# Kernel tuning notes

Measured on AMD Instinct MI355X. Metric: run time of the kernel, lower is better.

Reference implementation:

```python
import jax, jax.numpy as jnp
import numpy as np

R, C, N, E, H, F, ED, G, L = 1, 4, 50000, 200000, 128, 128, 16, 64, 2


def setup_inputs() -> dict:
    key = jax.random.key(0)
    ks = jax.random.split(key, 16)
    s = 0.05
    return {
        "x": jax.random.normal(ks[0], (R * C * N, H), jnp.float32),
        "batch": jnp.sort(jax.random.randint(ks[1], (N,), 0, G)),
        "edge_index": jax.random.randint(ks[2], (2, E), 0, N),
        "edge_attr": jax.random.normal(ks[3], (1, 1, E, ED), jnp.float32),
        "node_mask": jax.random.uniform(ks[4], (R, C, N, 1), jnp.float32),
        "edge_mask": jax.random.uniform(ks[5], (R, C, E, 1), jnp.float32),
        "W_be": jax.random.normal(ks[6], (ED, H), jnp.float32) * s,
        "b_be": jnp.zeros((H,), jnp.float32),
        "eps": jnp.zeros((L,), jnp.float32),
        "W1": jax.random.normal(ks[7], (L, H, H), jnp.float32) * s,
        "b1": jnp.zeros((L, H), jnp.float32),
        "W2": jax.random.normal(ks[8], (L, H, H), jnp.float32) * s,
        "b2": jnp.zeros((L, H), jnp.float32),
        "Wm1": jax.random.normal(ks[9], (H, H), jnp.float32) * s,
        "bm1": jnp.zeros((H,), jnp.float32),
        "Wm2": jax.random.normal(ks[10], (H, F), jnp.float32) * s,
        "bm2": jnp.zeros((F,), jnp.float32),
    }


def reference(x, batch, edge_index, edge_attr, node_mask, edge_mask,
              W_be, b_be, eps, W1, b1, W2, b2, Wm1, bm1, Wm2, bm2):
    gelu = lambda v: jax.nn.gelu(v, approximate=False)  # torch F.gelu default is erf
    src, dst = edge_index[0], edge_index[1]
    # bond encoder, shared across conv layers: (1,1,E,H)
    ee = edge_attr @ W_be + b_be
    for l in range(L):
        ux = x.reshape(R, C, N, H)
        # gather + add + GELU + edge-weight multiply: (R,C,E,H)
        msg = gelu(ux[:, :, src, :] + ee) * edge_mask
        # scatter_sum over edges into destination nodes
        agg = jnp.zeros_like(ux).at[:, :, dst, :].add(msg)
        h = (1.0 + eps[l]) * x + agg.reshape(x.shape)
        # conv MLP: Linear -> GELU -> Linear, then outer GELU (norm=Identity, dropout=0)
        h = gelu(h @ W1[l] + b1[l]) @ W2[l] + b2[l]
        x = gelu(h)
    # final node MLP (PyG MLP, norm=None): Linear -> GELU -> Linear
    x = gelu(x @ Wm1 + bm1) @ Wm2 + bm2  # (R*C*N, F)
    x4 = x.reshape(R, C, N, F)
    # masked mean-pool per (repeat, centroid, graph)
    num = jnp.zeros((R, C, G, F), x.dtype).at[:, :, batch, :].add(x4 * node_mask)
    den = jnp.zeros((R, C, G, 1), x.dtype).at[:, :, batch, :].add(node_mask) + 1e-7
    pooled = (num / den).transpose(0, 2, 1, 3).reshape(-1, F)  # (R*G*C, F)
    return pooled
```

## Files before the change

### kernel.cpp

```cpp
#include <hip/hip_runtime.h>
#include <math.h>

#define NN 50000
#define EN 200000
#define CC 4
#define HH 128
#define GG 64
#define LDSA 136
#define LDSF 132

typedef __attribute__((ext_vector_type(8))) short bs8;
typedef __attribute__((ext_vector_type(4))) float f32x4;
typedef __attribute__((ext_vector_type(2))) float f32x2;

__device__ __forceinline__ unsigned short f2bf(float f) {
  unsigned int u = __float_as_uint(f);
  u += 0x7FFFu + ((u >> 16) & 1u);
  return (unsigned short)(u >> 16);
}
__device__ __forceinline__ float bf2f(unsigned short h) {
  return __uint_as_float(((unsigned int)h) << 16);
}
__device__ __forceinline__ float gelu_f(float x) {
  float z = fabsf(x) * 0.7071067811865476f;
  float t = __builtin_amdgcn_rcpf(fmaf(0.3275911f, z, 1.0f));
  float poly = t * fmaf(t, fmaf(t, fmaf(t, fmaf(t, 1.061405429f, -1.453152027f),
                                        1.421413741f), -0.284496736f), 0.254829592f);
  float e = fmaf(-poly, __expf(-z * z), 1.0f);
  return 0.5f * x * (1.0f + copysignf(e, x));
}
__device__ __forceinline__ float gelu2_f(float x) {
  float z = fabsf(x) * 0.7071067811865476f;
  float t = __builtin_amdgcn_rcpf(fmaf(0.3275911f, z, 1.0f));
  float poly = t * fmaf(t, fmaf(t, fmaf(t, fmaf(t, 1.061405429f, -1.453152027f),
                                        1.421413741f), -0.284496736f), 0.254829592f);
  float e = fmaf(-poly, __expf(-z * z), 1.0f);
  return x * (1.0f + copysignf(e, x));
}

__global__ __launch_bounds__(256) void count_kernel(const int* __restrict__ dst,
                                                    int* __restrict__ counts) {
  int e = blockIdx.x * 256 + threadIdx.x;
  if (e < EN) atomicAdd(&counts[dst[e]], 1);
}

__global__ __launch_bounds__(256) void block_sum_kernel(const int* __restrict__ counts,
                                                        int* __restrict__ bsums) {
  int tid = threadIdx.x;
  int i = blockIdx.x * 256 + tid;
  int v = (i < NN) ? counts[i] : 0;
#pragma unroll
  for (int d = 1; d < 64; d <<= 1) v += __shfl_xor(v, d);
  __shared__ int ws4[4];
  if ((tid & 63) == 0) ws4[tid >> 6] = v;
  __syncthreads();
  if (tid == 0) bsums[blockIdx.x] = ws4[0] + ws4[1] + ws4[2] + ws4[3];
}

__global__ __launch_bounds__(256) void bsum_scan_kernel(const int* __restrict__ bsums,
                                                        int* __restrict__ boffs, int nb) {
  int tid = threadIdx.x, lane = tid & 63, wv = tid >> 6;
  int v = (tid < nb) ? bsums[tid] : 0;
  int s = v;
#pragma unroll
  for (int d = 1; d < 64; d <<= 1) { int t = __shfl_up(s, d); if (lane >= d) s += t; }
  __shared__ int wsum[4];
  if (lane == 63) wsum[wv] = s;
  __syncthreads();
  int pre = 0;
  for (int j = 0; j < wv; ++j) pre += wsum[j];
  if (tid < nb) boffs[tid] = pre + s - v;
}

__global__ __launch_bounds__(256) void block_scan_kernel(const int* __restrict__ counts,
                                                         const int* __restrict__ boffs,
                                                         int* __restrict__ offsets,
                                                         int* __restrict__ cursor) {
  int tid = threadIdx.x, lane = tid & 63, wv = tid >> 6;
  int i = blockIdx.x * 256 + tid;
  int v = (i < NN) ? counts[i] : 0;
  int s = v;
#pragma unroll
  for (int d = 1; d < 64; d <<= 1) { int t = __shfl_up(s, d); if (lane >= d) s += t; }
  __shared__ int wsum[4];
  if (lane == 63) wsum[wv] = s;
  __syncthreads();
  int pre = boffs[blockIdx.x];
  for (int j = 0; j < wv; ++j) pre += wsum[j];
  if (i < NN) { int e = pre + s - v; offsets[i] = e; cursor[i] = e; }
  if (i == 0) offsets[NN] = EN;
}

__global__ __launch_bounds__(256) void fill_kernel(const int* __restrict__ dst,
                                                   const int* __restrict__ src,
                                                   const float* __restrict__ emask,
                                                   int* __restrict__ cursor,
                                                   int2* __restrict__ csr_es,
                                                   float4* __restrict__ emask_s) {
  int e = blockIdx.x * 256 + threadIdx.x;
  if (e < EN) {
    int s = src[e];
    float m0 = emask[e];
    float m1 = emask[EN + e];
    float m2 = emask[2 * EN + e];
    float m3 = emask[3 * EN + e];
    int pos = atomicAdd(&cursor[dst[e]], 1);
    csr_es[pos] = make_int2(e, s);
    emask_s[pos] = make_float4(m0, m1, m2, m3);
  }
}

__global__ __launch_bounds__(256) void prep_w_kernel(const float* __restrict__ W1,
                                                     const float* __restrict__ W2,
                                                     const float* __restrict__ Wm1,
                                                     const float* __restrict__ Wm2,
                                                     unsigned short* __restrict__ wts) {
  int m = blockIdx.x >> 6;
  int idx = (blockIdx.x & 63) * 256 + threadIdx.x;
  const float* src = (m == 0) ? W1 : (m == 1) ? W1 + 16384 : (m == 2) ? W2
                     : (m == 3) ? W2 + 16384 : (m == 4) ? Wm1 : Wm2;
  unsigned short* dhi = wts + m * 32768;
  unsigned short* dlo = dhi + 16384;
  int n = idx >> 7, k = idx & 127;
  float v = src[k * HH + n];
  unsigned short hi = f2bf(v);
  dhi[n * HH + k] = hi;
  dlo[n * HH + k] = f2bf(v - bf2f(hi));
}

__global__ __launch_bounds__(256) void ee_kernel(const float* __restrict__ eattr,
                                                 const float* __restrict__ Wbe,
                                                 const float* __restrict__ bbe,
                                                 float* __restrict__ ee) {
  __shared__ float Ws[16 * HH];
  __shared__ float Ea[16 * 16];
  int tid = threadIdx.x;
  int e0 = blockIdx.x * 16;
#pragma unroll
  for (int i = 0; i < 8; ++i) Ws[tid + i * 256] = Wbe[tid + i * 256];
  Ea[tid] = eattr[(size_t)e0 * 16 + tid];
  __syncthreads();
  int h = tid & 127, half = tid >> 7;
  float bb = bbe[h];
#pragma unroll
  for (int j = 0; j < 8; ++j) {
    int el = j * 2 + half;
    float acc = bb;
#pragma unroll
    for (int d = 0; d < 16; ++d) acc += Ea[el * 16 + d] * Ws[d * HH + h];
    ee[(size_t)(e0 + el) * HH + h] = acc;
  }
}

__device__ __forceinline__ void loadW(const unsigned short* __restrict__ whi,
                                      const unsigned short* __restrict__ wlo,
                                      bs8 (&bh)[4][2], bs8 (&bl)[4][2],
                                      int ln, int quad, int wq) {
#pragma unroll
  for (int ks = 0; ks < 4; ++ks)
#pragma unroll
    for (int nt = 0; nt < 2; ++nt) {
      int wrow = ((wq * 2 + nt) * 16 + ln) * HH + ks * 32 + quad * 8;
      bh[ks][nt] = *(const bs8*)(whi + wrow);
      bl[ks][nt] = *(const bs8*)(wlo + wrow);
    }
}
__device__ __forceinline__ void zacc(f32x4 (&acc)[4][2]) {
#pragma unroll
  for (int mt = 0; mt < 4; ++mt)
#pragma unroll
    for (int nt = 0; nt < 2; ++nt)
#pragma unroll
      for (int r = 0; r < 4; ++r) acc[mt][nt][r] = 0.f;
}
__device__ __forceinline__ void gemm3(const unsigned short* Ahi, const unsigned short* Alo,
                                      const bs8 (&bh)[4][2], const bs8 (&bl)[4][2],
                                      f32x4 (&acc)[4][2], int ln, int quad) {
#pragma unroll
  for (int ks = 0; ks < 4; ++ks) {
    bs8 ah[4], al[4];
    int sb = ((ks * 4 + quad) ^ ln) * 8;
#pragma unroll
    for (int mt = 0; mt < 4; ++mt) {
      ah[mt] = *(const bs8*)(Ahi + (mt * 16 + ln) * HH + sb);
      al[mt] = *(const bs8*)(Alo + (mt * 16 + ln) * HH + sb);
    }
#pragma unroll
    for (int nt = 0; nt < 2; ++nt)
#pragma unroll
      for (int mt = 0; mt < 4; ++mt) {
        acc[mt][nt] = __builtin_amdgcn_mfma_f32_16x16x32_bf16(al[mt], bh[ks][nt], acc[mt][nt], 0, 0, 0);
        acc[mt][nt] = __builtin_amdgcn_mfma_f32_16x16x32_bf16(ah[mt], bl[ks][nt], acc[mt][nt], 0, 0, 0);
        acc[mt][nt] = __builtin_amdgcn_mfma_f32_16x16x32_bf16(ah[mt], bh[ks][nt], acc[mt][nt], 0, 0, 0);
      }
  }
}
__device__ __forceinline__ void tstage(unsigned short* Ahi, unsigned short* Alo,
                                       const float* __restrict__ b1v, f32x4 (&acc)[4][2],
                                       int ln, int quad, int wq) {
#pragma unroll
  for (int nt = 0; nt < 2; ++nt) {
    int col = (wq * 2 + nt) * 16 + ln;
    int cb = col >> 3, co = col & 7;
    float bb = b1v[col];
#pragma unroll
    for (int mt = 0; mt < 4; ++mt)
#pragma unroll
      for (int r = 0; r < 4; ++r) {
        float tv = gelu_f(acc[mt][nt][r] + bb);
        unsigned short th = f2bf(tv);
        int rr = mt * 16 + quad * 4 + r;
        int sof = rr * HH + (cb ^ (rr & 15)) * 8 + co;
        Ahi[sof] = th;
        Alo[sof] = f2bf(tv - bf2f(th));
      }
  }
}

__global__ __launch_bounds__(256, 4) void layer_kernel(
    const float* __restrict__ x,
    const float* __restrict__ ee,
    const int* __restrict__ off,
    const int2* __restrict__ csr_es,
    const float4* __restrict__ emask_s,
    const float* __restrict__ epsp, int layer,
    const unsigned short* __restrict__ w1hi, const unsigned short* __restrict__ w1lo,
    const float* __restrict__ b1,
    const unsigned short* __restrict__ w2hi, const unsigned short* __restrict__ w2lo,
    const float* __restrict__ b2,
    float* __restrict__ out) {
  __shared__ __align__(16) unsigned short AB[2 * 64 * HH];
  unsigned short* Ahi = AB;
  unsigned short* Alo = AB + 64 * HH;
  int tid = threadIdx.x;
  int lane = tid & 63, wq = tid >> 6;
  int ln = lane & 15, quad = lane >> 4;
  int n0 = blockIdx.x * 16;
  int c2 = lane * 2;
  float ep = 1.0f + epsp[layer];
  int blk = lane >> 2;
  int wo = (lane & 3) * 2;

  for (int j = 0; j < 4; ++j) {
    int nn = wq * 4 + j;
    int v = n0 + nn;
    float2 acc[CC];
#pragma unroll
    for (int c = 0; c < CC; ++c) { acc[c].x = 0.f; acc[c].y = 0.f; }
    int beg = off[v], end = off[v + 1];

    float2 eeC; float2 xC[CC]; float emC[CC];
    int2 esN = make_int2(0, 0);
    eeC.x = 0.f; eeC.y = 0.f;
#pragma unroll
    for (int c = 0; c < CC; ++c) { xC[c].x = 0.f; xC[c].y = 0.f; emC[c] = 0.f; }

    if (beg < end) {
      int2 es0 = csr_es[beg];
      eeC = *(const float2*)(ee + (size_t)es0.x * HH + c2);
#pragma unroll
      for (int c = 0; c < CC; ++c)
        xC[c] = *(const float2*)(x + ((size_t)c * NN + es0.y) * HH + c2);
      float4 m = emask_s[beg];
      emC[0] = 0.5f * m.x; emC[1] = 0.5f * m.y; emC[2] = 0.5f * m.z; emC[3] = 0.5f * m.w;
      if (beg + 1 < end) esN = csr_es[beg + 1];
    }

    for (int t = beg; t < end; ++t) {
      float2 eeB; float2 xB[CC]; float emB[CC];
      int2 esNN = make_int2(0, 0);
      if (t + 1 < end) {
        eeB = *(const float2*)(ee + (size_t)esN.x * HH + c2);
#pragma unroll
        for (int c = 0; c < CC; ++c)
          xB[c] = *(const float2*)(x + ((size_t)c * NN + esN.y) * HH + c2);
        float4 m = emask_s[t + 1];
        emB[0] = 0.5f * m.x; emB[1] = 0.5f * m.y; emB[2] = 0.5f * m.z; emB[3] = 0.5f * m.w;
        if (t + 2 < end) esNN = csr_es[t + 2];
      } else {
        eeB.x = 0.f; eeB.y = 0.f;
#pragma unroll
        for (int c = 0; c < CC; ++c) { xB[c].x = 0.f; xB[c].y = 0.f; emB[c] = 0.f; }
      }
#pragma unroll
      for (int c = 0; c < CC; ++c) {
        acc[c].x += gelu2_f(xC[c].x + eeC.x) * emC[c];
        acc[c].y += gelu2_f(xC[c].y + eeC.y) * emC[c];
      }
      eeC = eeB;
#pragma unroll
      for (int c = 0; c < CC; ++c) { xC[c] = xB[c]; emC[c] = emB[c]; }
      esN = esNN;
    }

#pragma unroll
    for (int c = 0; c < CC; ++c) {
      float2 xs = *(const float2*)(x + ((size_t)c * NN + v) * HH + c2);
      float o0 = fmaf(ep, xs.x, acc[c].x);
      float o1 = fmaf(ep, xs.y, acc[c].y);
      int rr = c * 16 + nn;
      int base = rr * HH + ((blk ^ (rr & 15)) * 8) + wo;
      unsigned short h0 = f2bf(o0), h1 = f2bf(o1);
      ushort2 hv; hv.x = h0; hv.y = h1;
      ushort2 lv; lv.x = f2bf(o0 - bf2f(h0)); lv.y = f2bf(o1 - bf2f(h1));
      *(ushort2*)(Ahi + base) = hv;
      *(ushort2*)(Alo + base) = lv;
    }
  }

  bs8 w1h[4][2], w1l[4][2];
  loadW(w1hi, w1lo, w1h, w1l, ln, quad, wq);
  __syncthreads();

  f32x4 acc[4][2];
  zacc(acc);
  gemm3(Ahi, Alo, w1h, w1l, acc, ln, quad);
  __syncthreads();

  bs8 w2h[4][2], w2l[4][2];
  loadW(w2hi, w2lo, w2h, w2l, ln, quad, wq);
  tstage(Ahi, Alo, b1, acc, ln, quad, wq);
  __syncthreads();

  zacc(acc);
  gemm3(Ahi, Alo, w2h, w2l, acc, ln, quad);

#pragma unroll
  for (int nt = 0; nt < 2; ++nt) {
    int col = (wq * 2 + nt) * 16 + ln;
    float bb = b2[col];
#pragma unroll
    for (int mt = 0; mt < 4; ++mt)
#pragma unroll
      for (int r = 0; r < 4; ++r) {
        float o = gelu_f(acc[mt][nt][r] + bb);
        out[((size_t)mt * NN + n0 + quad * 4 + r) * HH + col] = o;
      }
  }
}

__global__ __launch_bounds__(256, 2) void mlp_pool_kernel(
    const float* __restrict__ in,
    const unsigned short* __restrict__ w1hi, const unsigned short* __restrict__ w1lo,
    const float* __restrict__ b1,
    const unsigned short* __restrict__ w2hi, const unsigned short* __restrict__ w2lo,
    const float* __restrict__ b2,
    const float* __restrict__ nmask, const int* __restrict__ batch,
    float* __restrict__ num) {
  __shared__ __align__(16) unsigned short AB[128 * LDSA];
  __shared__ int kk[64];
  unsigned short* Ahi = AB;
  unsigned short* Alo = AB + 64 * LDSA;
  int tid = threadIdx.x;
  int row0 = blockIdx.x * 64;
  int lane = tid & 63, wq = tid >> 6;
  int ln = lane & 15, quad = lane >> 4;

  bs8 b1h[4][2], b1l[4][2];
  loadW(w1hi, w1lo, b1h, b1l, ln, quad, wq);
#pragma unroll
  for (int i = 0; i < 8; ++i) {
    int idx = tid + i * 256;
    int r = idx >> 5, cc4 = idx & 31;
    f32x4 vv = __builtin_nontemporal_load(
        (const f32x4*)(in + (size_t)(row0 + r) * HH + cc4 * 4));
    unsigned short h0 = f2bf(vv[0]), h1 = f2bf(vv[1]), h2 = f2bf(vv[2]), h3 = f2bf(vv[3]);
    ushort4 hv; hv.x = h0; hv.y = h1; hv.z = h2; hv.w = h3;
    ushort4 lv;
    lv.x = f2bf(vv[0] - bf2f(h0)); lv.y = f2bf(vv[1] - bf2f(h1));
    lv.z = f2bf(vv[2] - bf2f(h2)); lv.w = f2bf(vv[3] - bf2f(h3));
    *(ushort4*)(Ahi + r * LDSA + cc4 * 4) = hv;
    *(ushort4*)(Alo + r * LDSA + cc4 * 4) = lv;
  }
  if (tid < 64) {
    int gr = row0 + tid;
    int c = gr / NN;
    int n = gr - c * NN;
    kk[tid] = (c << 6) | batch[n];
  }
  __syncthreads();

  f32x4 acc[4][2];
  zacc(acc);
#pragma unroll
  for (int ks = 0; ks < 4; ++ks) {
    bs8 ah[4], al[4];
#pragma unroll
    for (int mt = 0; mt < 4; ++mt) {
      ah[mt] = *(const bs8*)(Ahi + (mt * 16 + ln) * LDSA + ks * 32 + quad * 8);
      al[mt] = *(const bs8*)(Alo + (mt * 16 + ln) * LDSA + ks * 32 + quad * 8);
    }
#pragma unroll
    for (int nt = 0; nt < 2; ++nt)
#pragma unroll
      for (int mt = 0; mt < 4; ++mt) {
        acc[mt][nt] = __builtin_amdgcn_mfma_f32_16x16x32_bf16(al[mt], b1h[ks][nt], acc[mt][nt], 0, 0, 0);
        acc[mt][nt] = __builtin_amdgcn_mfma_f32_16x16x32_bf16(ah[mt], b1l[ks][nt], acc[mt][nt], 0, 0, 0);
        acc[mt][nt] = __builtin_amdgcn_mfma_f32_16x16x32_bf16(ah[mt], b1h[ks][nt], acc[mt][nt], 0, 0, 0);
      }
  }
  __syncthreads();

  bs8 b2h[4][2], b2l[4][2];
  loadW(w2hi, w2lo, b2h, b2l, ln, quad, wq);
#pragma unroll
  for (int nt = 0; nt < 2; ++nt) {
    int col = (wq * 2 + nt) * 16 + ln;
    float bb = b1[col];
#pragma unroll
    for (int mt = 0; mt < 4; ++mt)
#pragma unroll
      for (int r = 0; r < 4; ++r) {
        float tv = gelu_f(acc[mt][nt][r] + bb);
        unsigned short th = f2bf(tv);
        int rr = mt * 16 + quad * 4 + r;
        Ahi[rr * LDSA + col] = th;
        Alo[rr * LDSA + col] = f2bf(tv - bf2f(th));
      }
  }
  __syncthreads();

  zacc(acc);
#pragma unroll
  for (int ks = 0; ks < 4; ++ks) {
    bs8 ah[4], al[4];
#pragma unroll
    for (int mt = 0; mt < 4; ++mt) {
      ah[mt] = *(const bs8*)(Ahi + (mt * 16 + ln) * LDSA + ks * 32 + quad * 8);
      al[mt] = *(const bs8*)(Alo + (mt * 16 + ln) * LDSA + ks * 32 + quad * 8);
    }
#pragma unroll
    for (int nt = 0; nt < 2; ++nt)
#pragma unroll
      for (int mt = 0; mt < 4; ++mt) {
        acc[mt][nt] = __builtin_amdgcn_mfma_f32_16x16x32_bf16(al[mt], b2h[ks][nt], acc[mt][nt], 0, 0, 0);
        acc[mt][nt] = __builtin_amdgcn_mfma_f32_16x16x32_bf16(ah[mt], b2l[ks][nt], acc[mt][nt], 0, 0, 0);
        acc[mt][nt] = __builtin_amdgcn_mfma_f32_16x16x32_bf16(ah[mt], b2h[ks][nt], acc[mt][nt], 0, 0, 0);
      }
  }
  __syncthreads();
  float* Tf = (float*)AB;
#pragma unroll
  for (int nt = 0; nt < 2; ++nt) {
    int col = (wq * 2 + nt) * 16 + ln;
    float bb = b2[col];
#pragma unroll
    for (int mt = 0; mt < 4; ++mt)
#pragma unroll
      for (int r = 0; r < 4; ++r) {
        int rl = mt * 16 + quad * 4 + r;
        int gr = row0 + rl;
        Tf[rl * LDSF + col] = (acc[mt][nt][r] + bb) * nmask[gr];
      }
  }
  __syncthreads();
  if (tid < 128) {
    int col = tid;
    float a2 = 0.f;
    int cur = kk[0];
    for (int r = 0; r < 64; ++r) {
      int k2 = kk[r];
      if (k2 != cur) {
        atomicAdd(&num[((size_t)(cur & 63) * CC + (cur >> 6)) * HH + col], a2);
        a2 = 0.f;
        cur = k2;
      }
      a2 += Tf[r * LDSF + col];
    }
    atomicAdd(&num[((size_t)(cur & 63) * CC + (cur >> 6)) * HH + col], a2);
  }
}

__global__ __launch_bounds__(256) void pool_finalize_kernel(const float* __restrict__ num,
                                                            const int* __restrict__ batch,
                                                            const float* __restrict__ nmask,
                                                            float* __restrict__ outp) {
  int g = blockIdx.x >> 2, c = blockIdx.x & 3;
  int lo = 0, hi = NN;
  while (lo < hi) { int m = (lo + hi) >> 1; if (batch[m] < g) lo = m + 1; else hi = m; }
  int start = lo;
  hi = NN;
  while (lo < hi) { int m = (lo + hi) >> 1; if (batch[m] < g + 1) lo = m + 1; else hi = m; }
  int end = lo;
  int tid = threadIdx.x;
  float d = 0.f;
  for (int n = start + tid; n < end; n += 256) d += nmask[c * NN + n];
#pragma unroll
  for (int k = 1; k < 64; k <<= 1) d += __shfl_xor(d, k);
  __shared__ float ws4[4];
  if ((tid & 63) == 0) ws4[tid >> 6] = d;
  __syncthreads();
  float den = ws4[0] + ws4[1] + ws4[2] + ws4[3] + 1e-7f;
  if (tid < 128) {
    int idx = blockIdx.x * 128 + tid;
    outp[idx] = num[idx] / den;
  }
}

extern "C" void kernel_launch(void* const* d_in, const int* in_sizes, int n_in,
                              void* d_out, int out_size, void* d_ws, size_t ws_size,
                              hipStream_t stream) {
  const float* x_in  = (const float*)d_in[0];
  const int*   batch = (const int*)d_in[1];
  const int*   eidx  = (const int*)d_in[2];
  const float* eattr = (const float*)d_in[3];
  const float* nmask = (const float*)d_in[4];
  const float* emask = (const float*)d_in[5];
  const float* Wbe   = (const float*)d_in[6];
  const float* bbe   = (const float*)d_in[7];
  const float* epsp  = (const float*)d_in[8];
  const float* W1    = (const float*)d_in[9];
  const float* b1    = (const float*)d_in[10];
  const float* W2    = (const float*)d_in[11];
  const float* b2    = (const float*)d_in[12];
  const float* Wm1   = (const float*)d_in[13];
  const float* bm1   = (const float*)d_in[14];
  const float* Wm2   = (const float*)d_in[15];
  const float* bm2   = (const float*)d_in[16];
  float* outp = (float*)d_out;

  const int* srcp = eidx;
  const int* dstp = eidx + EN;

  char* ws = (char*)d_ws;
  float* ee   = (float*)(ws);
  float* hbuf = (float*)(ws + 102400000);
  float* xbuf = (float*)(ws + 204800000);
  int* counts  = (int*)(ws + 307200000);
  int* offsets = (int*)(ws + 307400000);
  int* cursor  = (int*)(ws + 307600008);
  int2* csr_es = (int2*)(ws + 307800016);
  float4* emask_s = (float4*)(ws + 309400016);
  unsigned short* wts = (unsigned short*)(ws + 312600016);
  int* bsums = (int*)ws;
  int* boffs = (int*)(ws + 1024);
  float* num = (float*)ws;

  const int NB = (NN + 255) / 256;

  hipMemsetAsync(counts, 0, NN * sizeof(int), stream);
  count_kernel<<<(EN + 255) / 256, 256, 0, stream>>>(dstp, counts);
  block_sum_kernel<<<NB, 256, 0, stream>>>(counts, bsums);
  bsum_scan_kernel<<<1, 256, 0, stream>>>(bsums, boffs, NB);
  block_scan_kernel<<<NB, 256, 0, stream>>>(counts, boffs, offsets, cursor);
  fill_kernel<<<(EN + 255) / 256, 256, 0, stream>>>(dstp, srcp, emask, cursor, csr_es, emask_s);

  prep_w_kernel<<<384, 256, 0, stream>>>(W1, W2, Wm1, Wm2, wts);

  ee_kernel<<<EN / 16, 256, 0, stream>>>(eattr, Wbe, bbe, ee);

  layer_kernel<<<NN / 16, 256, 0, stream>>>(x_in, ee, offsets, csr_es, emask_s, epsp, 0,
                                            wts + 0, wts + 16384, b1,
                                            wts + 65536, wts + 81920, b2, hbuf);
  layer_kernel<<<NN / 16, 256, 0, stream>>>(hbuf, ee, offsets, csr_es, emask_s, epsp, 1,
                                            wts + 32768, wts + 49152, b1 + 128,
                                            wts + 98304, wts + 114688, b2 + 128, xbuf);
  hipMemsetAsync(num, 0, 131072, stream);
  mlp_pool_kernel<<<(CC * NN) / 64, 256, 0, stream>>>(xbuf, wts + 131072, wts + 147456, bm1,
                                                      wts + 163840, wts + 180224, bm2,
                                                      nmask, batch, num);
  pool_finalize_kernel<<<GG * CC, 256, 0, stream>>>(num, batch, nmask, outp);
}
```

Baseline: 678.5 us.

## Fuse second GIN layer with final node MLP and masked pooling

```diff
diff --git a/kernel.cpp b/kernel.cpp
--- a/kernel.cpp
+++ b/kernel.cpp
@@ -6,7 +6,6 @@
 #define CC 4
 #define HH 128
 #define GG 64
-#define LDSA 136
 #define LDSF 132
 
 typedef __attribute__((ext_vector_type(8))) short bs8;
@@ -196,13 +195,13 @@
   }
 }
 __device__ __forceinline__ void tstage(unsigned short* Ahi, unsigned short* Alo,
-                                       const float* __restrict__ b1v, f32x4 (&acc)[4][2],
+                                       const float* __restrict__ bv, f32x4 (&acc)[4][2],
                                        int ln, int quad, int wq) {
 #pragma unroll
   for (int nt = 0; nt < 2; ++nt) {
     int col = (wq * 2 + nt) * 16 + ln;
     int cb = col >> 3, co = col & 7;
-    float bb = b1v[col];
+    float bb = bv[col];
 #pragma unroll
     for (int mt = 0; mt < 4; ++mt)
 #pragma unroll
@@ -214,6 +213,85 @@
         Ahi[sof] = th;
         Alo[sof] = f2bf(tv - bf2f(th));
       }
+  }
+}
+
+__device__ __forceinline__ void agg_phase(const float* __restrict__ x,
+                                          const float* __restrict__ ee,
+                                          const int* __restrict__ off,
+                                          const int2* __restrict__ csr_es,
+                                          const float4* __restrict__ emask_s,
+                                          float ep, int n0,
+                                          unsigned short* Ahi, unsigned short* Alo,
+                                          int lane, int wq) {
+  int c2 = lane * 2;
+  int blk = lane >> 2;
+  int wo = (lane & 3) * 2;
+  for (int j = 0; j < 4; ++j) {
+    int nn = wq * 4 + j;
+    int v = n0 + nn;
+    float2 acc[CC];
+#pragma unroll
+    for (int c = 0; c < CC; ++c) { acc[c].x = 0.f; acc[c].y = 0.f; }
+    int beg = off[v], end = off[v + 1];
+
+    float2 eeC; float2 xC[CC]; float emC[CC];
+    int2 esN = make_int2(0, 0);
+    eeC.x = 0.f; eeC.y = 0.f;
+#pragma unroll
+    for (int c = 0; c < CC; ++c) { xC[c].x = 0.f; xC[c].y = 0.f; emC[c] = 0.f; }
+
+    if (beg < end) {
+      int2 es0 = csr_es[beg];
+      eeC = *(const float2*)(ee + (size_t)es0.x * HH + c2);
+#pragma unroll
+      for (int c = 0; c < CC; ++c)
+        xC[c] = *(const float2*)(x + ((size_t)c * NN + es0.y) * HH + c2);
+      float4 m = emask_s[beg];
+      emC[0] = 0.5f * m.x; emC[1] = 0.5f * m.y; emC[2] = 0.5f * m.z; emC[3] = 0.5f * m.w;
+      if (beg + 1 < end) esN = csr_es[beg + 1];
+    }
+
+    for (int t = beg; t < end; ++t) {
+      float2 eeB; float2 xB[CC]; float emB[CC];
+      int2 esNN = make_int2(0, 0);
+      if (t + 1 < end) {
+        eeB = *(const float2*)(ee + (size_t)esN.x * HH + c2);
+#pragma unroll
+        for (int c = 0; c < CC; ++c)
+          xB[c] = *(const float2*)(x + ((size_t)c * NN + esN.y) * HH + c2);
+        float4 m = emask_s[t + 1];
+        emB[0] = 0.5f * m.x; emB[1] = 0.5f * m.y; emB[2] = 0.5f * m.z; emB[3] = 0.5f * m.w;
+        if (t + 2 < end) esNN = csr_es[t + 2];
+      } else {
+        eeB.x = 0.f; eeB.y = 0.f;
+#pragma unroll
+        for (int c = 0; c < CC; ++c) { xB[c].x = 0.f; xB[c].y = 0.f; emB[c] = 0.f; }
+      }
+#pragma unroll
+      for (int c = 0; c < CC; ++c) {
+        acc[c].x += gelu2_f(xC[c].x + eeC.x) * emC[c];
+        acc[c].y += gelu2_f(xC[c].y + eeC.y) * emC[c];
+      }
+      eeC = eeB;
+#pragma unroll
+      for (int c = 0; c < CC; ++c) { xC[c] = xB[c]; emC[c] = emB[c]; }
+      esN = esNN;
+    }
+
+#pragma unroll
+    for (int c = 0; c < CC; ++c) {
+      float2 xs = *(const float2*)(x + ((size_t)c * NN + v) * HH + c2);
+      float o0 = fmaf(ep, xs.x, acc[c].x);
+      float o1 = fmaf(ep, xs.y, acc[c].y);
+      int rr = c * 16 + nn;
+      int base = rr * HH + ((blk ^ (rr & 15)) * 8) + wo;
+      unsigned short h0 = f2bf(o0), h1 = f2bf(o1);
+      ushort2 hv; hv.x = h0; hv.y = h1;
+      ushort2 lv; lv.x = f2bf(o0 - bf2f(h0)); lv.y = f2bf(o1 - bf2f(h1));
+      *(ushort2*)(Ahi + base) = hv;
+      *(ushort2*)(Alo + base) = lv;
+    }
   }
 }
 
@@ -236,77 +314,8 @@
   int lane = tid & 63, wq = tid >> 6;
   int ln = lane & 15, quad = lane >> 4;
   int n0 = blockIdx.x * 16;
-  int c2 = lane * 2;
-  float ep = 1.0f + epsp[layer];
-  int blk = lane >> 2;
-  int wo = (lane & 3) * 2;
-
-  for (int j = 0; j < 4; ++j) {
-    int nn = wq * 4 + j;
-    int v = n0 + nn;
-    float2 acc[CC];
-#pragma unroll
-    for (int c = 0; c < CC; ++c) { acc[c].x = 0.f; acc[c].y = 0.f; }
-    int beg = off[v], end = off[v + 1];
-
-    float2 eeC; float2 xC[CC]; float emC[CC];
-    int2 esN = make_int2(0, 0);
-    eeC.x = 0.f; eeC.y = 0.f;
-#pragma unroll
-    for (int c = 0; c < CC; ++c) { xC[c].x = 0.f; xC[c].y = 0.f; emC[c] = 0.f; }
-
-    if (beg < end) {
-      int2 es0 = csr_es[beg];
-      eeC = *(const float2*)(ee + (size_t)es0.x * HH + c2);
-#pragma unroll
-      for (int c = 0; c < CC; ++c)
-        xC[c] = *(const float2*)(x + ((size_t)c * NN + es0.y) * HH + c2);
-      float4 m = emask_s[beg];
-      emC[0] = 0.5f * m.x; emC[1] = 0.5f * m.y; emC[2] = 0.5f * m.z; emC[3] = 0.5f * m.w;
-      if (beg + 1 < end) esN = csr_es[beg + 1];
-    }
-
-    for (int t = beg; t < end; ++t) {
-      float2 eeB; float2 xB[CC]; float emB[CC];
-      int2 esNN = make_int2(0, 0);
-      if (t + 1 < end) {
-        eeB = *(const float2*)(ee + (size_t)esN.x * HH + c2);
-#pragma unroll
-        for (int c = 0; c < CC; ++c)
-          xB[c] = *(const float2*)(x + ((size_t)c * NN + esN.y) * HH + c2);
-        float4 m = emask_s[t + 1];
-        emB[0] = 0.5f * m.x; emB[1] = 0.5f * m.y; emB[2] = 0.5f * m.z; emB[3] = 0.5f * m.w;
-        if (t + 2 < end) esNN = csr_es[t + 2];
-      } else {
-        eeB.x = 0.f; eeB.y = 0.f;
-#pragma unroll
-        for (int c = 0; c < CC; ++c) { xB[c].x = 0.f; xB[c].y = 0.f; emB[c] = 0.f; }
-      }
-#pragma unroll
-      for (int c = 0; c < CC; ++c) {
-        acc[c].x += gelu2_f(xC[c].x + eeC.x) * emC[c];
-        acc[c].y += gelu2_f(xC[c].y + eeC.y) * emC[c];
-      }
-      eeC = eeB;
-#pragma unroll
-      for (int c = 0; c < CC; ++c) { xC[c] = xB[c]; emC[c] = emB[c]; }
-      esN = esNN;
-    }
-
-#pragma unroll
-    for (int c = 0; c < CC; ++c) {
-      float2 xs = *(const float2*)(x + ((size_t)c * NN + v) * HH + c2);
-      float o0 = fmaf(ep, xs.x, acc[c].x);
-      float o1 = fmaf(ep, xs.y, acc[c].y);
-      int rr = c * 16 + nn;
-      int base = rr * HH + ((blk ^ (rr & 15)) * 8) + wo;
-      unsigned short h0 = f2bf(o0), h1 = f2bf(o1);
-      ushort2 hv; hv.x = h0; hv.y = h1;
-      ushort2 lv; lv.x = f2bf(o0 - bf2f(h0)); lv.y = f2bf(o1 - bf2f(h1));
-      *(ushort2*)(Ahi + base) = hv;
-      *(ushort2*)(Alo + base) = lv;
-    }
-  }
+
+  agg_phase(x, ee, off, csr_es, emask_s, 1.0f + epsp[layer], n0, Ahi, Alo, lane, wq);
 
   bs8 w1h[4][2], w1l[4][2];
   loadW(w1hi, w1lo, w1h, w1l, ln, quad, wq);
@@ -339,118 +348,83 @@
   }
 }
 
-__global__ __launch_bounds__(256, 2) void mlp_pool_kernel(
-    const float* __restrict__ in,
+__global__ __launch_bounds__(256, 4) void layer_pool_kernel(
+    const float* __restrict__ x,
+    const float* __restrict__ ee,
+    const int* __restrict__ off,
+    const int2* __restrict__ csr_es,
+    const float4* __restrict__ emask_s,
+    const float* __restrict__ epsp, int layer,
     const unsigned short* __restrict__ w1hi, const unsigned short* __restrict__ w1lo,
     const float* __restrict__ b1,
     const unsigned short* __restrict__ w2hi, const unsigned short* __restrict__ w2lo,
     const float* __restrict__ b2,
+    const unsigned short* __restrict__ m1hi, const unsigned short* __restrict__ m1lo,
+    const float* __restrict__ bm1,
+    const unsigned short* __restrict__ m2hi, const unsigned short* __restrict__ m2lo,
+    const float* __restrict__ bm2,
     const float* __restrict__ nmask, const int* __restrict__ batch,
     float* __restrict__ num) {
-  __shared__ __align__(16) unsigned short AB[128 * LDSA];
+  __shared__ __align__(16) unsigned short AB[64 * LDSF * 2];
   __shared__ int kk[64];
   unsigned short* Ahi = AB;
-  unsigned short* Alo = AB + 64 * LDSA;
+  unsigned short* Alo = AB + 64 * HH;
   int tid = threadIdx.x;
-  int row0 = blockIdx.x * 64;
   int lane = tid & 63, wq = tid >> 6;
   int ln = lane & 15, quad = lane >> 4;
-
-  bs8 b1h[4][2], b1l[4][2];
-  loadW(w1hi, w1lo, b1h, b1l, ln, quad, wq);
-#pragma unroll
-  for (int i = 0; i < 8; ++i) {
-    int idx = tid + i * 256;
-    int r = idx >> 5, cc4 = idx & 31;
-    f32x4 vv = __builtin_nontemporal_load(
-        (const f32x4*)(in + (size_t)(row0 + r) * HH + cc4 * 4));
-    unsigned short h0 = f2bf(vv[0]), h1 = f2bf(vv[1]), h2 = f2bf(vv[2]), h3 = f2bf(vv[3]);
-    ushort4 hv; hv.x = h0; hv.y = h1; hv.z = h2; hv.w = h3;
-    ushort4 lv;
-    lv.x = f2bf(vv[0] - bf2f(h0)); lv.y = f2bf(vv[1] - bf2f(h1));
-    lv.z = f2bf(vv[2] - bf2f(h2)); lv.w = f2bf(vv[3] - bf2f(h3));
-    *(ushort4*)(Ahi + r * LDSA + cc4 * 4) = hv;
-    *(ushort4*)(Alo + r * LDSA + cc4 * 4) = lv;
-  }
+  int n0 = blockIdx.x * 16;
+
   if (tid < 64) {
-    int gr = row0 + tid;
-    int c = gr / NN;
-    int n = gr - c * NN;
-    kk[tid] = (c << 6) | batch[n];
-  }
+    int c = tid >> 4, nn = tid & 15;
+    kk[tid] = (c << 6) | batch[n0 + nn];
+  }
+
+  agg_phase(x, ee, off, csr_es, emask_s, 1.0f + epsp[layer], n0, Ahi, Alo, lane, wq);
+
+  bs8 wh[4][2], wl[4][2];
+  loadW(w1hi, w1lo, wh, wl, ln, quad, wq);
   __syncthreads();
 
   f32x4 acc[4][2];
   zacc(acc);
-#pragma unroll
-  for (int ks = 0; ks < 4; ++ks) {
-    bs8 ah[4], al[4];
-#pragma unroll
-    for (int mt = 0; mt < 4; ++mt) {
-      ah[mt] = *(const bs8*)(Ahi + (mt * 16 + ln) * LDSA + ks * 32 + quad * 8);
-      al[mt] = *(const bs8*)(Alo + (mt * 16 + ln) * LDSA + ks * 32 + quad * 8);
-    }
-#pragma unroll
-    for (int nt = 0; nt < 2; ++nt)
-#pragma unroll
-      for (int mt = 0; mt < 4; ++mt) {
-        acc[mt][nt] = __builtin_amdgcn_mfma_f32_16x16x32_bf16(al[mt], b1h[ks][nt], acc[mt][nt], 0, 0, 0);
-        acc[mt][nt] = __builtin_amdgcn_mfma_f32_16x16x32_bf16(ah[mt], b1l[ks][nt], acc[mt][nt], 0, 0, 0);
-        acc[mt][nt] = __builtin_amdgcn_mfma_f32_16x16x32_bf16(ah[mt], b1h[ks][nt], acc[mt][nt], 0, 0, 0);
-      }
-  }
-  __syncthreads();
-
-  bs8 b2h[4][2], b2l[4][2];
-  loadW(w2hi, w2lo, b2h, b2l, ln, quad, wq);
+  gemm3(Ahi, Alo, wh, wl, acc, ln, quad);
+  __syncthreads();
+
+  loadW(w2hi, w2lo, wh, wl, ln, quad, wq);
+  tstage(Ahi, Alo, b1, acc, ln, quad, wq);
+  __syncthreads();
+
+  zacc(acc);
+  gemm3(Ahi, Alo, wh, wl, acc, ln, quad);
+  __syncthreads();
+
+  loadW(m1hi, m1lo, wh, wl, ln, quad, wq);
+  tstage(Ahi, Alo, b2, acc, ln, quad, wq);
+  __syncthreads();
+
+  zacc(acc);
+  gemm3(Ahi, Alo, wh, wl, acc, ln, quad);
+  __syncthreads();
+
+  loadW(m2hi, m2lo, wh, wl, ln, quad, wq);
+  tstage(Ahi, Alo, bm1, acc, ln, quad, wq);
+  __syncthreads();
+
+  zacc(acc);
+  gemm3(Ahi, Alo, wh, wl, acc, ln, quad);
+  __syncthreads();
+
+  float* Tf = (float*)AB;
 #pragma unroll
   for (int nt = 0; nt < 2; ++nt) {
     int col = (wq * 2 + nt) * 16 + ln;
-    float bb = b1[col];
-#pragma unroll
-    for (int mt = 0; mt < 4; ++mt)
-#pragma unroll
-      for (int r = 0; r < 4; ++r) {
-        float tv = gelu_f(acc[mt][nt][r] + bb);
-        unsigned short th = f2bf(tv);
-        int rr = mt * 16 + quad * 4 + r;
-        Ahi[rr * LDSA + col] = th;
-        Alo[rr * LDSA + col] = f2bf(tv - bf2f(th));
-      }
-  }
-  __syncthreads();
-
-  zacc(acc);
-#pragma unroll
-  for (int ks = 0; ks < 4; ++ks) {
-    bs8 ah[4], al[4];
-#pragma unroll
-    for (int mt = 0; mt < 4; ++mt) {
-      ah[mt] = *(const bs8*)(Ahi + (mt * 16 + ln) * LDSA + ks * 32 + quad * 8);
-      al[mt] = *(const bs8*)(Alo + (mt * 16 + ln) * LDSA + ks * 32 + quad * 8);
-    }
-#pragma unroll
-    for (int nt = 0; nt < 2; ++nt)
-#pragma unroll
-      for (int mt = 0; mt < 4; ++mt) {
-        acc[mt][nt] = __builtin_amdgcn_mfma_f32_16x16x32_bf16(al[mt], b2h[ks][nt], acc[mt][nt], 0, 0, 0);
-        acc[mt][nt] = __builtin_amdgcn_mfma_f32_16x16x32_bf16(ah[mt], b2l[ks][nt], acc[mt][nt], 0, 0, 0);
-        acc[mt][nt] = __builtin_amdgcn_mfma_f32_16x16x32_bf16(ah[mt], b2h[ks][nt], acc[mt][nt], 0, 0, 0);
-      }
-  }
-  __syncthreads();
-  float* Tf = (float*)AB;
-#pragma unroll
-  for (int nt = 0; nt < 2; ++nt) {
-    int col = (wq * 2 + nt) * 16 + ln;
-    float bb = b2[col];
+    float bb = bm2[col];
 #pragma unroll
     for (int mt = 0; mt < 4; ++mt)
 #pragma unroll
       for (int r = 0; r < 4; ++r) {
         int rl = mt * 16 + quad * 4 + r;
-        int gr = row0 + rl;
-        Tf[rl * LDSF + col] = (acc[mt][nt][r] + bb) * nmask[gr];
+        Tf[rl * LDSF + col] = (acc[mt][nt][r] + bb) * nmask[(size_t)mt * NN + n0 + quad * 4 + r];
       }
   }
   __syncthreads();
@@ -525,7 +499,7 @@
   char* ws = (char*)d_ws;
   float* ee   = (float*)(ws);
   float* hbuf = (float*)(ws + 102400000);
-  float* xbuf = (float*)(ws + 204800000);
+  float* num  = (float*)(ws + 204800000);
   int* counts  = (int*)(ws + 307200000);
   int* offsets = (int*)(ws + 307400000);
   int* cursor  = (int*)(ws + 307600008);
@@ -534,7 +508,6 @@
   unsigned short* wts = (unsigned short*)(ws + 312600016);
   int* bsums = (int*)ws;
   int* boffs = (int*)(ws + 1024);
-  float* num = (float*)ws;
 
   const int NB = (NN + 255) / 256;
 
@@ -549,15 +522,16 @@
 
   ee_kernel<<<EN / 16, 256, 0, stream>>>(eattr, Wbe, bbe, ee);
 
+  hipMemsetAsync(num, 0, 131072, stream);
+
   layer_kernel<<<NN / 16, 256, 0, stream>>>(x_in, ee, offsets, csr_es, emask_s, epsp, 0,
                                             wts + 0, wts + 16384, b1,
                                             wts + 65536, wts + 81920, b2, hbuf);
-  layer_kernel<<<NN / 16, 256, 0, stream>>>(hbuf, ee, offsets, csr_es, emask_s, epsp, 1,
-                                            wts + 32768, wts + 49152, b1 + 128,
-                                            wts + 98304, wts + 114688, b2 + 128, xbuf);
-  hipMemsetAsync(num, 0, 131072, stream);
-  mlp_pool_kernel<<<(CC * NN) / 64, 256, 0, stream>>>(xbuf, wts + 131072, wts + 147456, bm1,
-                                                      wts + 163840, wts + 180224, bm2,
-                                                      nmask, batch, num);
+  layer_pool_kernel<<<NN / 16, 256, 0, stream>>>(hbuf, ee, offsets, csr_es, emask_s, epsp, 1,
+                                                 wts + 32768, wts + 49152, b1 + 128,
+                                                 wts + 98304, wts + 114688, b2 + 128,
+                                                 wts + 131072, wts + 147456, bm1,
+                                                 wts + 163840, wts + 180224, bm2,
+                                                 nmask, batch, num);
   pool_finalize_kernel<<<GG * CC, 256, 0, stream>>>(num, batch, nmask, outp);
 }
```

Measured after the change: 688.7 us. Within noise of the previous version (+1.5%).

## Distribute block edges across waves with LDS atomic accumulation for load balance

Applied to the files above, without the earlier changes.

```diff
diff --git a/kernel.cpp b/kernel.cpp
--- a/kernel.cpp
+++ b/kernel.cpp
@@ -95,17 +95,18 @@
                                                    const int* __restrict__ src,
                                                    const float* __restrict__ emask,
                                                    int* __restrict__ cursor,
-                                                   int2* __restrict__ csr_es,
+                                                   int4* __restrict__ csr_esd,
                                                    float4* __restrict__ emask_s) {
   int e = blockIdx.x * 256 + threadIdx.x;
   if (e < EN) {
     int s = src[e];
+    int d = dst[e];
     float m0 = emask[e];
     float m1 = emask[EN + e];
     float m2 = emask[2 * EN + e];
     float m3 = emask[3 * EN + e];
-    int pos = atomicAdd(&cursor[dst[e]], 1);
-    csr_es[pos] = make_int2(e, s);
+    int pos = atomicAdd(&cursor[d], 1);
+    csr_esd[pos] = make_int4(e, s, d, 0);
     emask_s[pos] = make_float4(m0, m1, m2, m3);
   }
 }
@@ -196,13 +197,13 @@
   }
 }
 __device__ __forceinline__ void tstage(unsigned short* Ahi, unsigned short* Alo,
-                                       const float* __restrict__ b1v, f32x4 (&acc)[4][2],
+                                       const float* __restrict__ bv, f32x4 (&acc)[4][2],
                                        int ln, int quad, int wq) {
 #pragma unroll
   for (int nt = 0; nt < 2; ++nt) {
     int col = (wq * 2 + nt) * 16 + ln;
     int cb = col >> 3, co = col & 7;
-    float bb = b1v[col];
+    float bb = bv[col];
 #pragma unroll
     for (int mt = 0; mt < 4; ++mt)
 #pragma unroll
@@ -217,11 +218,81 @@
   }
 }
 
+__device__ __forceinline__ void agg_phase(const float* __restrict__ x,
+                                          const float* __restrict__ ee,
+                                          const int* __restrict__ off,
+                                          const int4* __restrict__ csr_esd,
+                                          const float4* __restrict__ emask_s,
+                                          float ep, int n0,
+                                          unsigned short* AB16, int tid) {
+  float* accf = (float*)AB16;
+  unsigned short* Ahi = AB16;
+  unsigned short* Alo = AB16 + 64 * HH;
+  int lane = tid & 63, wq = tid >> 6;
+
+#pragma unroll
+  for (int i = 0; i < 16; ++i)
+    *(float2*)&accf[(i * 256 + tid) * 2] = make_float2(0.f, 0.f);
+  __syncthreads();
+
+  int beg = off[n0], end = off[n0 + 16];
+  for (int t = beg + wq; t < end; t += 4) {
+    int4 esd = csr_esd[t];
+    float4 m = emask_s[t];
+    const float* eerow = ee + (size_t)esd.x * HH;
+    float ee0 = eerow[lane];
+    float ee1 = eerow[lane + 64];
+    int dl = esd.z - n0;
+    float m0 = 0.5f * m.x, m1 = 0.5f * m.y, m2 = 0.5f * m.z, m3 = 0.5f * m.w;
+    const float* x0r = x + ((size_t)0 * NN + esd.y) * HH;
+    const float* x1r = x + ((size_t)1 * NN + esd.y) * HH;
+    const float* x2r = x + ((size_t)2 * NN + esd.y) * HH;
+    const float* x3r = x + ((size_t)3 * NN + esd.y) * HH;
+    atomicAdd(&accf[(0 * 16 + dl) * HH + lane],      gelu2_f(x0r[lane] + ee0) * m0);
+    atomicAdd(&accf[(0 * 16 + dl) * HH + lane + 64], gelu2_f(x0r[lane + 64] + ee1) * m0);
+    atomicAdd(&accf[(1 * 16 + dl) * HH + lane],      gelu2_f(x1r[lane] + ee0) * m1);
+    atomicAdd(&accf[(1 * 16 + dl) * HH + lane + 64], gelu2_f(x1r[lane + 64] + ee1) * m1);
+    atomicAdd(&accf[(2 * 16 + dl) * HH + lane],      gelu2_f(x2r[lane] + ee0) * m2);
+    atomicAdd(&accf[(2 * 16 + dl) * HH + lane + 64], gelu2_f(x2r[lane + 64] + ee1) * m2);
+    atomicAdd(&accf[(3 * 16 + dl) * HH + lane],      gelu2_f(x3r[lane] + ee0) * m3);
+    atomicAdd(&accf[(3 * 16 + dl) * HH + lane + 64], gelu2_f(x3r[lane + 64] + ee1) * m3);
+  }
+  __syncthreads();
+
+  float a0[16], a1[16];
+#pragma unroll
+  for (int i = 0; i < 16; ++i) {
+    int idx = i * 256 + tid;
+    int rr = idx >> 6, cw = idx & 63;
+    a0[i] = accf[rr * HH + cw];
+    a1[i] = accf[rr * HH + cw + 64];
+  }
+  __syncthreads();
+#pragma unroll
+  for (int i = 0; i < 16; ++i) {
+    int idx = i * 256 + tid;
+    int rr = idx >> 6, cw = idx & 63;
+    int c = rr >> 4, node = n0 + (rr & 15);
+    const float* xrow = x + ((size_t)c * NN + node) * HH;
+    float h0 = fmaf(ep, xrow[cw], a0[i]);
+    float h1 = fmaf(ep, xrow[cw + 64], a1[i]);
+    unsigned short hh0 = f2bf(h0), hh1 = f2bf(h1);
+    int swz = rr & 15;
+    int cw2 = cw + 64;
+    int off0 = rr * HH + (((cw >> 3) ^ swz) * 8) + (cw & 7);
+    int off1 = rr * HH + (((cw2 >> 3) ^ swz) * 8) + (cw2 & 7);
+    Ahi[off0] = hh0;
+    Alo[off0] = f2bf(h0 - bf2f(hh0));
+    Ahi[off1] = hh1;
+    Alo[off1] = f2bf(h1 - bf2f(hh1));
+  }
+}
+
 __global__ __launch_bounds__(256, 4) void layer_kernel(
     const float* __restrict__ x,
     const float* __restrict__ ee,
     const int* __restrict__ off,
-    const int2* __restrict__ csr_es,
+    const int4* __restrict__ csr_esd,
     const float4* __restrict__ emask_s,
     const float* __restrict__ epsp, int layer,
     const unsigned short* __restrict__ w1hi, const unsigned short* __restrict__ w1lo,
@@ -236,77 +307,8 @@
   int lane = tid & 63, wq = tid >> 6;
   int ln = lane & 15, quad = lane >> 4;
   int n0 = blockIdx.x * 16;
-  int c2 = lane * 2;
-  float ep = 1.0f + epsp[layer];
-  int blk = lane >> 2;
-  int wo = (lane & 3) * 2;
-
-  for (int j = 0; j < 4; ++j) {
-    int nn = wq * 4 + j;
-    int v = n0 + nn;
-    float2 acc[CC];
-#pragma unroll
-    for (int c = 0; c < CC; ++c) { acc[c].x = 0.f; acc[c].y = 0.f; }
-    int beg = off[v], end = off[v + 1];
-
-    float2 eeC; float2 xC[CC]; float emC[CC];
-    int2 esN = make_int2(0, 0);
-    eeC.x = 0.f; eeC.y = 0.f;
-#pragma unroll
-    for (int c = 0; c < CC; ++c) { xC[c].x = 0.f; xC[c].y = 0.f; emC[c] = 0.f; }
-
-    if (beg < end) {
-      int2 es0 = csr_es[beg];
-      eeC = *(const float2*)(ee + (size_t)es0.x * HH + c2);
-#pragma unroll
-      for (int c = 0; c < CC; ++c)
-        xC[c] = *(const float2*)(x + ((size_t)c * NN + es0.y) * HH + c2);
-      float4 m = emask_s[beg];
-      emC[0] = 0.5f * m.x; emC[1] = 0.5f * m.y; emC[2] = 0.5f * m.z; emC[3] = 0.5f * m.w;
-      if (beg + 1 < end) esN = csr_es[beg + 1];
-    }
-
-    for (int t = beg; t < end; ++t) {
-      float2 eeB; float2 xB[CC]; float emB[CC];
-      int2 esNN = make_int2(0, 0);
-      if (t + 1 < end) {
-        eeB = *(const float2*)(ee + (size_t)esN.x * HH + c2);
-#pragma unroll
-        for (int c = 0; c < CC; ++c)
-          xB[c] = *(const float2*)(x + ((size_t)c * NN + esN.y) * HH + c2);
-        float4 m = emask_s[t + 1];
-        emB[0] = 0.5f * m.x; emB[1] = 0.5f * m.y; emB[2] = 0.5f * m.z; emB[3] = 0.5f * m.w;
-        if (t + 2 < end) esNN = csr_es[t + 2];
-      } else {
-        eeB.x = 0.f; eeB.y = 0.f;
-#pragma unroll
-        for (int c = 0; c < CC; ++c) { xB[c].x = 0.f; xB[c].y = 0.f; emB[c] = 0.f; }
-      }
-#pragma unroll
-      for (int c = 0; c < CC; ++c) {
-        acc[c].x += gelu2_f(xC[c].x + eeC.x) * emC[c];
-        acc[c].y += gelu2_f(xC[c].y + eeC.y) * emC[c];
-      }
-      eeC = eeB;
-#pragma unroll
-      for (int c = 0; c < CC; ++c) { xC[c] = xB[c]; emC[c] = emB[c]; }
-      esN = esNN;
-    }
-
-#pragma unroll
-    for (int c = 0; c < CC; ++c) {
-      float2 xs = *(const float2*)(x + ((size_t)c * NN + v) * HH + c2);
-      float o0 = fmaf(ep, xs.x, acc[c].x);
-      float o1 = fmaf(ep, xs.y, acc[c].y);
-      int rr = c * 16 + nn;
-      int base = rr * HH + ((blk ^ (rr & 15)) * 8) + wo;
-      unsigned short h0 = f2bf(o0), h1 = f2bf(o1);
-      ushort2 hv; hv.x = h0; hv.y = h1;
-      ushort2 lv; lv.x = f2bf(o0 - bf2f(h0)); lv.y = f2bf(o1 - bf2f(h1));
-      *(ushort2*)(Ahi + base) = hv;
-      *(ushort2*)(Alo + base) = lv;
-    }
-  }
+
+  agg_phase(x, ee, off, csr_esd, emask_s, 1.0f + epsp[layer], n0, AB, tid);
 
   bs8 w1h[4][2], w1l[4][2];
   loadW(w1hi, w1lo, w1h, w1l, ln, quad, wq);
@@ -529,9 +531,9 @@
   int* counts  = (int*)(ws + 307200000);
   int* offsets = (int*)(ws + 307400000);
   int* cursor  = (int*)(ws + 307600008);
-  int2* csr_es = (int2*)(ws + 307800016);
-  float4* emask_s = (float4*)(ws + 309400016);
-  unsigned short* wts = (unsigned short*)(ws + 312600016);
+  int4* csr_esd = (int4*)(ws + 307800016);
+  float4* emask_s = (float4*)(ws + 311000016);
+  unsigned short* wts = (unsigned short*)(ws + 314200016);
   int* bsums = (int*)ws;
   int* boffs = (int*)(ws + 1024);
   float* num = (float*)ws;
@@ -543,16 +545,16 @@
   block_sum_kernel<<<NB, 256, 0, stream>>>(counts, bsums);
   bsum_scan_kernel<<<1, 256, 0, stream>>>(bsums, boffs, NB);
   block_scan_kernel<<<NB, 256, 0, stream>>>(counts, boffs, offsets, cursor);
-  fill_kernel<<<(EN + 255) / 256, 256, 0, stream>>>(dstp, srcp, emask, cursor, csr_es, emask_s);
+  fill_kernel<<<(EN + 255) / 256, 256, 0, stream>>>(dstp, srcp, emask, cursor, csr_esd, emask_s);
 
   prep_w_kernel<<<384, 256, 0, stream>>>(W1, W2, Wm1, Wm2, wts);
 
   ee_kernel<<<EN / 16, 256, 0, stream>>>(eattr, Wbe, bbe, ee);
 
-  layer_kernel<<<NN / 16, 256, 0, stream>>>(x_in, ee, offsets, csr_es, emask_s, epsp, 0,
+  layer_kernel<<<NN / 16, 256, 0, stream>>>(x_in, ee, offsets, csr_esd, emask_s, epsp, 0,
                                             wts + 0, wts + 16384, b1,
                                             wts + 65536, wts + 81920, b2, hbuf);
-  layer_kernel<<<NN / 16, 256, 0, stream>>>(hbuf, ee, offsets, csr_es, emask_s, epsp, 1,
+  layer_kernel<<<NN / 16, 256, 0, stream>>>(hbuf, ee, offsets, csr_esd, emask_s, epsp, 1,
                                             wts + 32768, wts + 49152, b1 + 128,
                                             wts + 98304, wts + 114688, b2 + 128, xbuf);
   hipMemsetAsync(num, 0, 131072, stream);
```

Result: slower. 1.495 ms (+120.4%).
